# Performance work log

Measured on AMD Instinct MI355X. Metric: run time of the kernel, lower is better.

## Reference

```python
import jax, jax.numpy as jnp
import numpy as np

NB = 5  # frequency bands


def _ln(x, g, b, eps=1e-5):
    m = jnp.mean(x, axis=-1, keepdims=True)
    v = jnp.var(x, axis=-1, keepdims=True)
    return (x - m) / jnp.sqrt(v + eps) * g + b


def _graph_adj(x, adj_w, sw1, sb1, sw2, sb2, pos_factor, pos_enc):
    # x: [B, D, N] -> degree-normalized adjacency [B, N, N]
    d = x.shape[1]
    xt = jnp.swapaxes(x, 1, 2)  # [B, N, D]
    # concat-MLP first layer split: cat(xi, xj) @ W1 == xi @ W1[:d] + xj @ W1[d:]
    a = xt @ sw1[:d]
    bpart = xt @ sw1[d:]
    h = jax.nn.elu(a[:, :, None, :] + bpart[:, None, :, :] + sb1)  # [B, N, N, H]
    dyn = jax.nn.sigmoid(jnp.squeeze(h @ sw2, -1) + sb2)  # [B, N, N]
    static = jax.nn.softmax(adj_w, axis=-1)
    pos = jax.nn.softmax(pos_enc, axis=-1)
    comb = jax.nn.softmax(static + dyn + pos_factor * pos, axis=-1)
    deg = jnp.sum(comb, axis=-1)
    dis = (deg + 1e-8) ** -0.5
    return dis[:, :, None] * comb * dis[:, None, :]


def _gcn(x, adj, w, b):
    # x: [B, D, N], adj: [B, N, N] -> [B, D_out, N]
    xt = jnp.swapaxes(x, 1, 2)
    out = jnp.einsum('bij,bjd->bid', adj, xt) @ w + b
    return jnp.swapaxes(out, 1, 2)


def _mha(x, qkv_w, qkv_b, ow, ob, nh=4):
    B, S, D = x.shape
    dh = D // nh
    q, k, v = jnp.split(x @ qkv_w + qkv_b, 3, axis=-1)
    q = q.reshape(B, S, nh, dh)
    k = k.reshape(B, S, nh, dh)
    v = v.reshape(B, S, nh, dh)
    att = jax.nn.softmax(jnp.einsum('bihd,bjhd->bhij', q, k) / float(np.sqrt(dh)), axis=-1)
    o = jnp.einsum('bhij,bjhd->bihd', att, v).reshape(B, S, D)
    return o @ ow + ob


def setup_inputs():
    key = jax.random.key(0)
    B, D, N = 16, 256, 64
    ks = iter(jax.random.split(key, 40))

    def rn(shape, s=0.05):
        return jax.random.normal(next(ks), shape, dtype=jnp.float32) * s

    eyeN = jnp.eye(N, dtype=jnp.float32)
    return dict(
        feature=jax.random.normal(next(ks), (B, NB * D, 1, N), dtype=jnp.float32),
        l_adj_w=jnp.tile(eyeN[None], (NB, 1, 1)),
        l_sim_w1=rn((NB, 2 * D, D)), l_sim_b1=jnp.zeros((NB, D), jnp.float32),
        l_sim_w2=rn((NB, D, 1)), l_sim_b2=jnp.zeros((NB, 1), jnp.float32),
        l_pos_factor=jnp.full((NB,), 0.5, jnp.float32),
        l_pos_enc=jnp.tile(eyeN[None], (NB, 1, 1)),
        l_gcn_w=rn((NB, D, D)), l_gcn_b=jnp.zeros((NB, D), jnp.float32),
        g_adj_w=jnp.eye(NB, dtype=jnp.float32),
        g_sim_w1=rn((2 * D, D)), g_sim_b1=jnp.zeros((D,), jnp.float32),
        g_sim_w2=rn((D, 1)), g_sim_b2=jnp.zeros((1,), jnp.float32),
        g_pos_factor=jnp.float32(0.5),
        g_pos_enc=jnp.eye(NB, dtype=jnp.float32),
        g_gcn_w=rn((D, D)), g_gcn_b=jnp.zeros((D,), jnp.float32),
        qkv_w=rn((D, 3 * D)), qkv_b=jnp.zeros((3 * D,), jnp.float32),
        attn_ow=rn((D, D)), attn_ob=jnp.zeros((D,), jnp.float32),
        ln1_g=jnp.ones((D,), jnp.float32), ln1_b=jnp.zeros((D,), jnp.float32),
        ln2_g=jnp.ones((D,), jnp.float32), ln2_b=jnp.zeros((D,), jnp.float32),
        mlp_w1=rn((D, 4 * D)), mlp_b1=jnp.zeros((4 * D,), jnp.float32),
        mlp_w2=rn((4 * D, D)), mlp_b2=jnp.zeros((D,), jnp.float32),
        imp_w=rn((NB, N, 1)), imp_b=jnp.zeros((NB, 1), jnp.float32),
    )


def reference(feature, l_adj_w, l_sim_w1, l_sim_b1, l_sim_w2, l_sim_b2,
              l_pos_factor, l_pos_enc, l_gcn_w, l_gcn_b,
              g_adj_w, g_sim_w1, g_sim_b1, g_sim_w2, g_sim_b2,
              g_pos_factor, g_pos_enc, g_gcn_w, g_gcn_b,
              qkv_w, qkv_b, attn_ow, attn_ob,
              ln1_g, ln1_b, ln2_g, ln2_b,
              mlp_w1, mlp_b1, mlp_w2, mlp_b2,
              imp_w, imp_b):
    B = feature.shape[0]
    D = l_gcn_w.shape[-1]
    N = feature.shape[-1]
    # [B, 5*D, 1, N] -> [5, B, D, N] band-major
    x5 = jnp.moveaxis(feature.reshape(B, NB, D, N), 1, 0)
    # per-band local graphs + GCNs (vmapped over the 5 bands)
    local_adj = jax.vmap(_graph_adj)(x5, l_adj_w, l_sim_w1, l_sim_b1,
                                     l_sim_w2, l_sim_b2, l_pos_factor, l_pos_enc)
    local_out = jax.vmap(_gcn)(x5, local_adj, l_gcn_w, l_gcn_b)  # [5, B, D, N]
    scale_nodes = jnp.moveaxis(jnp.mean(local_out, axis=-1), 0, 1)  # [B, 5, D]
    # cross-band attention block (pre: MHA + residual + LN, then MLP + residual + LN)
    attn = _mha(scale_nodes, qkv_w, qkv_b, attn_ow, attn_ob)
    h1 = _ln(scale_nodes + attn, ln1_g, ln1_b)
    mlp = jax.nn.gelu(h1 @ mlp_w1 + mlp_b1, approximate=False) @ mlp_w2 + mlp_b2
    se = _ln(h1 + mlp, ln2_g, ln2_b)  # [B, 5, D]
    # global scale graph over the 5 band nodes
    xg = jnp.swapaxes(se, 1, 2)  # [B, D, 5]
    g_adj = _graph_adj(xg, g_adj_w, g_sim_w1, g_sim_b1, g_sim_w2, g_sim_b2,
                       g_pos_factor, g_pos_enc)
    g_out = jnp.swapaxes(_gcn(xg, g_adj, g_gcn_w, g_gcn_b), 1, 2)  # [B, 5, D]
    # modulate each local band feature by its global scale vector
    enh = local_out * jnp.moveaxis(g_out, 1, 0)[..., None]  # [5, B, D, N]
    # per-band importance projection over channels: [5, B, D, 1]
    out5 = jnp.einsum('kbdn,kno->kbdo', enh, imp_w) + imp_b[:, None, None, :]
    output = jnp.moveaxis(out5, 0, 1).reshape(B, NB * D, 1, 1)
    return output, g_adj, jnp.moveaxis(local_out, 0, 1)
```

## Files before the change

### kernel.cpp

```cpp
#include <hip/hip_runtime.h>
#include <hip/hip_bf16.h>

#define NBANDS 5
#define BATCH  16
#define DIM    256
#define NNODE  64
#define SEQ    5
#define NHEAD  4
#define DHEAD  64

typedef __hip_bfloat16 bf16;
typedef unsigned short ushort_t;
typedef __attribute__((ext_vector_type(8))) short short8;
typedef __attribute__((ext_vector_type(4))) float float4v;

__device__ __forceinline__ float bu2f(ushort_t u){
    bf16 h = *reinterpret_cast<bf16*>(&u);
    return __bfloat162float(h);
}
__device__ __forceinline__ ushort_t f2bu(float x){
    bf16 h = __float2bfloat16(x);
    return *reinterpret_cast<ushort_t*>(&h);
}

__global__ void __launch_bounds__(256) k_head(
    const float* __restrict__ l_adj_w, const float* __restrict__ l_pos_enc,
    const float* __restrict__ l_pf,
    const float* __restrict__ g_adj_w, const float* __restrict__ g_pos_enc,
    const float* __restrict__ g_pf,
    float* __restrict__ sbase, float* __restrict__ gbase,
    const float* __restrict__ w1, const float* __restrict__ gw,
    ushort_t* __restrict__ w1bt, ushort_t* __restrict__ gwbt,
    const float* __restrict__ feat,
    ushort_t* __restrict__ xtb, ushort_t* __restrict__ xtT)
{
    int blk = blockIdx.x;
    int tid = threadIdx.x;
    __shared__ ushort_t tile[64][65];

    if (blk < 80) {
        int r = blk*4 + (tid>>6);
        int k = r >> 6, i = r & 63;
        int t = tid & 63;
        float aw = l_adj_w[(k*NNODE + i)*NNODE + t];
        float pe = l_pos_enc[(k*NNODE + i)*NNODE + t];
        float m1 = aw, m2 = pe;
        for (int o=32;o>0;o>>=1){ m1 = fmaxf(m1, __shfl_xor(m1,o,64)); m2 = fmaxf(m2, __shfl_xor(m2,o,64)); }
        float e1 = __expf(aw-m1), e2 = __expf(pe-m2);
        float s1=e1, s2=e2;
        for (int o=32;o>0;o>>=1){ s1 += __shfl_xor(s1,o,64); s2 += __shfl_xor(s2,o,64); }
        float pf = l_pf[k];
        sbase[(k*NNODE+i)*NNODE + t] = e1/s1 + pf*(e2/s2);
    } else if (blk == 80) {
        if (tid < NBANDS) {
            int i = tid;
            float r1[NBANDS], r2[NBANDS];
            float m1=-1e30f, m2=-1e30f;
            for (int j=0;j<NBANDS;j++){
                r1[j]=g_adj_w[i*NBANDS+j]; r2[j]=g_pos_enc[i*NBANDS+j];
                m1=fmaxf(m1,r1[j]); m2=fmaxf(m2,r2[j]);
            }
            float s1=0.f,s2=0.f;
            for (int j=0;j<NBANDS;j++){ r1[j]=__expf(r1[j]-m1); r2[j]=__expf(r2[j]-m2); s1+=r1[j]; s2+=r2[j]; }
            float pf = g_pf[0];
            for (int j=0;j<NBANDS;j++) gbase[i*NBANDS+j] = r1[j]/s1 + pf*(r2[j]/s2);
        }
    } else if (blk < 321) {
        int idx = blk - 81;
        int inst = idx >> 4;
        int t = idx & 15;
        int r0 = (t>>2)*64, c0 = (t&3)*64;
        const float* src; ushort_t* dst;
        if (inst < 10){
            int k = inst>>1, half = inst&1;
            src = w1  + ((size_t)k*512 + half*256)*256;
            dst = w1bt+ ((size_t)k*512 + half*256)*256;
        } else {
            int k = inst-10;
            src = gw  + (size_t)k*65536;
            dst = gwbt+ (size_t)k*65536;
        }
        int jj = tid & 63, i4 = tid >> 6;
        for (int p=0;p<16;p++){
            int i = p*4 + i4;
            tile[i][jj] = f2bu(src[(size_t)(r0+i)*256 + c0 + jj]);
        }
        __syncthreads();
        for (int p=0;p<16;p++){
            int i = p*4 + i4;
            dst[(size_t)(c0+i)*256 + r0 + jj] = tile[jj][i];
        }
    } else {
        int idx = blk - 321;
        int k = idx >> 6;
        int b = (idx >> 2) & 15;
        int dt = idx & 3;
        const float* src = feat + ((size_t)b*NBANDS*DIM + (size_t)k*DIM)*NNODE;
        ushort_t* dst = xtb + (size_t)(k*BATCH+b)*NNODE*DIM;
        ushort_t* dstT = xtT + (size_t)(k*BATCH+b)*DIM*NNODE;
        for (int u=0; u<16; ++u){
            int i = dt*4096 + u*256 + tid;
            dstT[i] = f2bu(src[i]);
        }
        for (int r=0;r<16;r++){
            int dp = r*4 + (tid>>6);
            int n  = tid & 63;
            tile[dp][n] = f2bu(src[(size_t)(dt*64+dp)*NNODE + n]);
        }
        __syncthreads();
        for (int r=0;r<16;r++){
            int n  = r*4 + (tid>>6);
            int dp = tid & 63;
            dst[(size_t)n*DIM + dt*64 + dp] = tile[dp][n];
        }
    }
}

__global__ void __launch_bounds__(256) k_ab_mfma(const ushort_t* __restrict__ xtb,
                        const ushort_t* __restrict__ w1bt, const float* __restrict__ b1,
                        ushort_t* __restrict__ aab, ushort_t* __restrict__ bbb)
{
    int blk = blockIdx.x;
    int kband = blk / (BATCH*8);
    int b = (blk/8) % BATCH;
    int nblk = blk & 7;
    int tid = threadIdx.x;
    int wave = tid>>6, lane = tid&63;
    int c16 = lane & 15, quad = lane >> 4;
    int m0 = wave*16;
    size_t rowbase = (size_t)(kband*BATCH+b)*NNODE;
    const ushort_t* Aptr = xtb + (rowbase + m0 + c16)*DIM + quad*8;
    const ushort_t* Bbase = w1bt + (size_t)kband*512*DIM;
    int ncol0 = nblk*64;
    const ushort_t* Bptr0 = Bbase + (size_t)(ncol0 +  0 + c16)*DIM + quad*8;
    const ushort_t* Bptr1 = Bbase + (size_t)(ncol0 + 16 + c16)*DIM + quad*8;
    const ushort_t* Bptr2 = Bbase + (size_t)(ncol0 + 32 + c16)*DIM + quad*8;
    const ushort_t* Bptr3 = Bbase + (size_t)(ncol0 + 48 + c16)*DIM + quad*8;
    float4v acc0 = {0.f,0.f,0.f,0.f}, acc1 = acc0, acc2 = acc0, acc3 = acc0;
    #pragma unroll
    for (int ks=0; ks<8; ++ks){
        short8 a  = *reinterpret_cast<const short8*>(Aptr  + ks*32);
        short8 b0 = *reinterpret_cast<const short8*>(Bptr0 + ks*32);
        short8 b1v= *reinterpret_cast<const short8*>(Bptr1 + ks*32);
        short8 b2 = *reinterpret_cast<const short8*>(Bptr2 + ks*32);
        short8 b3 = *reinterpret_cast<const short8*>(Bptr3 + ks*32);
        acc0 = __builtin_amdgcn_mfma_f32_16x16x32_bf16(a, b0, acc0, 0,0,0);
        acc1 = __builtin_amdgcn_mfma_f32_16x16x32_bf16(a, b1v, acc1, 0,0,0);
        acc2 = __builtin_amdgcn_mfma_f32_16x16x32_bf16(a, b2, acc2, 0,0,0);
        acc3 = __builtin_amdgcn_mfma_f32_16x16x32_bf16(a, b3, acc3, 0,0,0);
    }
    int half = nblk >> 2;
    int cbase = (nblk & 3)*64;
    ushort_t* dst = half ? bbb : aab;
    float4v accs[4] = {acc0, acc1, acc2, acc3};
    #pragma unroll
    for (int nt=0; nt<4; ++nt){
        int cg = cbase + nt*16 + c16;
        float bias = half ? 0.f : b1[kband*DIM + cg];
        #pragma unroll
        for (int r=0;r<4;r++){
            int m = m0 + quad*4 + r;
            dst[(rowbase + m)*DIM + cg] = f2bu(accs[nt][r] + bias);
        }
    }
}

__global__ void __launch_bounds__(256) k_dyn_comb(const ushort_t* __restrict__ aab,
                           const ushort_t* __restrict__ bbb,
                           const float* __restrict__ w2, const float* __restrict__ b2arr,
                           const float* __restrict__ sbase,
                           ushort_t* __restrict__ combb)
{
    int blk = blockIdx.x;
    int k = blk / (BATCH*16);
    int b = (blk / 16) % BATCH;
    int i0 = (blk % 16) * 4;
    int kb = k*BATCH + b;
    __shared__ ushort_t bs[64][260];
    __shared__ float arows[4][DIM];
    __shared__ float w2s[DIM];
    int tid = threadIdx.x;
    int wave = tid >> 6, lane = tid & 63;
    const ushort_t* bsrc = bbb + (size_t)kb*NNODE*DIM;
    for (int u=0; u<16; ++u){
        int idx = u*1024 + tid*4;
        int row = idx >> 8, col = idx & 255;
        *reinterpret_cast<ushort4*>(&bs[row][col]) =
            *reinterpret_cast<const ushort4*>(&bsrc[(size_t)row*DIM + col]);
    }
    for (int r=0;r<4;r++) arows[r][tid] = bu2f(aab[((size_t)kb*NNODE + i0 + r)*DIM + tid]);
    w2s[tid] = w2[k*DIM + tid];
    __syncthreads();

    int i = i0 + wave;
    float acc = 0.f;
    #pragma unroll 4
    for (int dd=0; dd<64; ++dd){
        ushort4 bv = *reinterpret_cast<const ushort4*>(&bs[lane][dd*4]);
        float4 av = *reinterpret_cast<const float4*>(&arows[wave][dd*4]);
        float4 wv = *reinterpret_cast<const float4*>(&w2s[dd*4]);
        float v0 = av.x + bu2f(bv.x);
        float v1 = av.y + bu2f(bv.y);
        float v2 = av.z + bu2f(bv.z);
        float v3 = av.w + bu2f(bv.w);
        float e0 = (v0>0.f)? v0 : (__expf(v0)-1.f);
        float e1 = (v1>0.f)? v1 : (__expf(v1)-1.f);
        float e2 = (v2>0.f)? v2 : (__expf(v2)-1.f);
        float e3 = (v3>0.f)? v3 : (__expf(v3)-1.f);
        acc += e0*wv.x + e1*wv.y + e2*wv.z + e3*wv.w;
    }
    float sb2 = b2arr[k];
    float sg = 1.f/(1.f + __expf(-(acc + sb2)));
    float val = sbase[(k*NNODE + i)*NNODE + lane] + sg;
    float m = val;
    for (int o=32;o>0;o>>=1) m = fmaxf(m, __shfl_xor(m,o,64));
    float e = __expf(val - m);
    float s = e;
    for (int o=32;o>0;o>>=1) s += __shfl_xor(s,o,64);
    combb[((size_t)kb*NNODE + i)*NNODE + lane] = f2bu(e/s);
}

__global__ void __launch_bounds__(256) k_y_mfma(const ushort_t* __restrict__ combb,
                       const ushort_t* __restrict__ xtT,
                       ushort_t* __restrict__ yb)
{
    int blk = blockIdx.x;
    int kband = blk / (BATCH*4);
    int b = (blk/4) % BATCH;
    int nblk = blk & 3;
    int tid = threadIdx.x;
    int wave = tid>>6, lane = tid&63;
    int c16 = lane & 15, quad = lane >> 4;
    int m0 = wave*16;
    int kb = kband*BATCH + b;
    const ushort_t* Aptr = combb + ((size_t)kb*NNODE + m0 + c16)*NNODE + quad*8;
    const ushort_t* Bbase = xtT + (size_t)kb*DIM*NNODE;
    int ncol0 = nblk*64;
    const ushort_t* Bptr0 = Bbase + (size_t)(ncol0 +  0 + c16)*NNODE + quad*8;
    const ushort_t* Bptr1 = Bbase + (size_t)(ncol0 + 16 + c16)*NNODE + quad*8;
    const ushort_t* Bptr2 = Bbase + (size_t)(ncol0 + 32 + c16)*NNODE + quad*8;
    const ushort_t* Bptr3 = Bbase + (size_t)(ncol0 + 48 + c16)*NNODE + quad*8;
    float4v acc0 = {0.f,0.f,0.f,0.f}, acc1 = acc0, acc2 = acc0, acc3 = acc0;
    #pragma unroll
    for (int ks=0; ks<2; ++ks){
        short8 a  = *reinterpret_cast<const short8*>(Aptr  + ks*32);
        short8 b0 = *reinterpret_cast<const short8*>(Bptr0 + ks*32);
        short8 b1v= *reinterpret_cast<const short8*>(Bptr1 + ks*32);
        short8 b2 = *reinterpret_cast<const short8*>(Bptr2 + ks*32);
        short8 b3 = *reinterpret_cast<const short8*>(Bptr3 + ks*32);
        acc0 = __builtin_amdgcn_mfma_f32_16x16x32_bf16(a, b0, acc0, 0,0,0);
        acc1 = __builtin_amdgcn_mfma_f32_16x16x32_bf16(a, b1v, acc1, 0,0,0);
        acc2 = __builtin_amdgcn_mfma_f32_16x16x32_bf16(a, b2, acc2, 0,0,0);
        acc3 = __builtin_amdgcn_mfma_f32_16x16x32_bf16(a, b3, acc3, 0,0,0);
    }
    size_t rowbase = (size_t)kb*NNODE;
    float4v accs[4] = {acc0, acc1, acc2, acc3};
    #pragma unroll
    for (int nt=0; nt<4; ++nt){
        int cg = ncol0 + nt*16 + c16;
        #pragma unroll
        for (int r=0;r<4;r++){
            int m = m0 + quad*4 + r;
            yb[(rowbase + m)*DIM + cg] = f2bu(accs[nt][r]);
        }
    }
}

__global__ void __launch_bounds__(256) k_gcn_mfma(const ushort_t* __restrict__ yb,
                         const ushort_t* __restrict__ gwbt, const float* __restrict__ gb,
                         const float* __restrict__ imp_w,
                         float* __restrict__ out_local,
                         float* __restrict__ scalew, float* __restrict__ impw)
{
    int blk = blockIdx.x;
    int kband = blk / (BATCH*4);
    int b = (blk/4) % BATCH;
    int nblk = blk & 3;
    int tid = threadIdx.x;
    int wave = tid>>6, lane = tid&63;
    int c16 = lane & 15, quad = lane >> 4;
    int m0 = wave*16;
    int kb = kband*BATCH + b;
    __shared__ float iw_s[NNODE];
    __shared__ float sred[4][64];
    __shared__ float ired[4][64];
    if (tid < NNODE) iw_s[tid] = imp_w[kband*NNODE + tid];
    const ushort_t* Aptr = yb + ((size_t)kb*NNODE + m0 + c16)*DIM + quad*8;
    const ushort_t* Bbase = gwbt + (size_t)kband*DIM*DIM;
    int ncol0 = nblk*64;
    const ushort_t* Bptr0 = Bbase + (size_t)(ncol0 +  0 + c16)*DIM + quad*8;
    const ushort_t* Bptr1 = Bbase + (size_t)(ncol0 + 16 + c16)*DIM + quad*8;
    const ushort_t* Bptr2 = Bbase + (size_t)(ncol0 + 32 + c16)*DIM + quad*8;
    const ushort_t* Bptr3 = Bbase + (size_t)(ncol0 + 48 + c16)*DIM + quad*8;
    float4v acc0 = {0.f,0.f,0.f,0.f}, acc1 = acc0, acc2 = acc0, acc3 = acc0;
    #pragma unroll
    for (int ks=0; ks<8; ++ks){
        short8 a  = *reinterpret_cast<const short8*>(Aptr  + ks*32);
        short8 b0 = *reinterpret_cast<const short8*>(Bptr0 + ks*32);
        short8 b1v= *reinterpret_cast<const short8*>(Bptr1 + ks*32);
        short8 b2 = *reinterpret_cast<const short8*>(Bptr2 + ks*32);
        short8 b3 = *reinterpret_cast<const short8*>(Bptr3 + ks*32);
        acc0 = __builtin_amdgcn_mfma_f32_16x16x32_bf16(a, b0, acc0, 0,0,0);
        acc1 = __builtin_amdgcn_mfma_f32_16x16x32_bf16(a, b1v, acc1, 0,0,0);
        acc2 = __builtin_amdgcn_mfma_f32_16x16x32_bf16(a, b2, acc2, 0,0,0);
        acc3 = __builtin_amdgcn_mfma_f32_16x16x32_bf16(a, b3, acc3, 0,0,0);
    }
    __syncthreads();
    float4v accs[4] = {acc0, acc1, acc2, acc3};
    #pragma unroll
    for (int nt=0; nt<4; ++nt){
        int cg = ncol0 + nt*16 + c16;
        float bias = gb[kband*DIM + cg];
        float v0 = accs[nt][0]+bias, v1 = accs[nt][1]+bias, v2 = accs[nt][2]+bias, v3 = accs[nt][3]+bias;
        float4 v = make_float4(v0, v1, v2, v3);
        float* dst = out_local + ((size_t)(b*NBANDS + kband)*DIM + cg)*NNODE + m0 + quad*4;
        *reinterpret_cast<float4*>(dst) = v;
        int nb = m0 + quad*4;
        float s  = v0 + v1 + v2 + v3;
        float di = v0*iw_s[nb] + v1*iw_s[nb+1] + v2*iw_s[nb+2] + v3*iw_s[nb+3];
        s  += __shfl_xor(s, 16, 64);  s  += __shfl_xor(s, 32, 64);
        di += __shfl_xor(di, 16, 64); di += __shfl_xor(di, 32, 64);
        if (quad == 0){
            sred[wave][nt*16 + c16] = s;
            ired[wave][nt*16 + c16] = di;
        }
    }
    __syncthreads();
    if (tid < 64){
        float s  = sred[0][tid] + sred[1][tid] + sred[2][tid] + sred[3][tid];
        float di = ired[0][tid] + ired[1][tid] + ired[2][tid] + ired[3][tid];
        size_t o = ((size_t)b*SEQ + kband)*DIM + ncol0 + tid;
        scalew[o] = s * (1.f/64.f);
        impw[o]   = di;
    }
}

template<int COLS, int SLICES>
__global__ void __launch_bounds__(256) k_gemv(const float* __restrict__ x, const float* __restrict__ w,
                       const float* __restrict__ bias, float* __restrict__ out,
                       int K, int N, int act)
{
    int chunks = N / COLS;
    int row = blockIdx.x / chunks;
    int n0 = (blockIdx.x % chunks) * COLS;
    int c = threadIdx.x % COLS, s = threadIdx.x / COLS;
    __shared__ float xs[1024];
    __shared__ float part[SLICES][COLS];
    for (int i = threadIdx.x; i < K; i += 256) xs[i] = x[(size_t)row*K + i];
    __syncthreads();
    int klen = K / SLICES;
    const float* wp = w + (size_t)(s*klen)*N + n0 + c;
    const float* xp = xs + s*klen;
    float acc = 0.f;
    #pragma unroll 8
    for (int i = 0; i < klen; ++i) acc += xp[i] * wp[(size_t)i*N];
    part[s][c] = acc;
    __syncthreads();
    if (s == 0){
        float v = bias[n0+c];
        #pragma unroll
        for (int q=0;q<SLICES;q++) v += part[q][c];
        if (act) v = 0.5f*v*(1.f + erff(v*0.70710678118654752f));
        out[(size_t)row*N + n0 + c] = v;
    }
}

__global__ void __launch_bounds__(256) k_projattn(const float* __restrict__ qkvw,
                        const float* __restrict__ ow, const float* __restrict__ ob,
                        float* __restrict__ projw)
{
    int row = blockIdx.x / 4;
    int n0 = (blockIdx.x % 4) * 64;
    int b = row / SEQ, i = row % SEQ;
    int tid = threadIdx.x;
    int h = tid >> 6, l = tid & 63;
    __shared__ float xs[DIM];
    __shared__ float part[4][64];
    const float* base = qkvw + (size_t)b*SEQ*3*DIM;
    float qv = base[(size_t)i*3*DIM + h*DHEAD + l];
    float pj[SEQ];
    #pragma unroll
    for (int j=0;j<SEQ;j++){
        float p = qv * base[(size_t)j*3*DIM + DIM + h*DHEAD + l];
        for (int o=32;o>0;o>>=1) p += __shfl_xor(p,o,64);
        pj[j] = p * 0.125f;
    }
    float m = pj[0];
    #pragma unroll
    for (int j=1;j<SEQ;j++) m = fmaxf(m, pj[j]);
    float ssum = 0.f;
    #pragma unroll
    for (int j=0;j<SEQ;j++){ pj[j] = __expf(pj[j]-m); ssum += pj[j]; }
    float inv = 1.f/ssum;
    float o = 0.f;
    #pragma unroll
    for (int j=0;j<SEQ;j++) o += pj[j]*inv * base[(size_t)j*3*DIM + 2*DIM + h*DHEAD + l];
    xs[tid] = o;
    __syncthreads();
    int c = tid & 63, s = tid >> 6;
    const float* wp = ow + (size_t)(s*64)*DIM + n0 + c;
    const float* xp = xs + s*64;
    float acc = 0.f;
    #pragma unroll 8
    for (int k=0;k<64;++k) acc += xp[k] * wp[(size_t)k*DIM];
    part[s][c] = acc;
    __syncthreads();
    if (s == 0){
        projw[(size_t)row*DIM + n0 + c] = ob[n0+c] + part[0][c]+part[1][c]+part[2][c]+part[3][c];
    }
}

__device__ __forceinline__ float block_ln(float v, int tid, float* red, float g, float bln)
{
    float s = v;
    for (int o=32;o>0;o>>=1) s += __shfl_xor(s,o,64);
    int wave = tid>>6, lane = tid&63;
    if (lane==0) red[wave] = s;
    __syncthreads();
    float mean = (red[0]+red[1]+red[2]+red[3]) * (1.f/DIM);
    float c = v - mean;
    float q = c*c;
    for (int o=32;o>0;o>>=1) q += __shfl_xor(q,o,64);
    __syncthreads();
    if (lane==0) red[wave] = q;
    __syncthreads();
    float var = (red[0]+red[1]+red[2]+red[3]) * (1.f/DIM);
    return c * rsqrtf(var + 1e-5f) * g + bln;
}

__global__ void __launch_bounds__(256) k_mlp1_ln(const float* __restrict__ projw,
                         const float* __restrict__ scalew,
                         const float* __restrict__ ln1_g, const float* __restrict__ ln1_b,
                         const float* __restrict__ w1, const float* __restrict__ b1,
                         float* __restrict__ h1w, float* __restrict__ mhw)
{
    int row = blockIdx.x / 16;
    int n0 = (blockIdx.x % 16) * 64;
    int tid = threadIdx.x;
    __shared__ float xs[DIM];
    __shared__ float red[4];
    __shared__ float part[4][64];
    float v = projw[(size_t)row*DIM + tid] + scalew[(size_t)row*DIM + tid];
    float h = block_ln(v, tid, red, ln1_g[tid], ln1_b[tid]);
    xs[tid] = h;
    if ((blockIdx.x % 16) == 0) h1w[(size_t)row*DIM + tid] = h;
    __syncthreads();
    int c = tid & 63, s = tid >> 6;
    const float* wp = w1 + (size_t)(s*64)*1024 + n0 + c;
    const float* xp = xs + s*64;
    float acc = 0.f;
    #pragma unroll 8
    for (int i=0;i<64;++i) acc += xp[i] * wp[(size_t)i*1024];
    part[s][c] = acc;
    __syncthreads();
    if (s == 0){
        float o = b1[n0+c] + part[0][c] + part[1][c] + part[2][c] + part[3][c];
        o = 0.5f*o*(1.f + erff(o*0.70710678118654752f));
        mhw[(size_t)row*1024 + n0 + c] = o;
    }
}

__global__ void __launch_bounds__(256) k_gab_ln(const float* __restrict__ m2w,
                        const float* __restrict__ h1w,
                        const float* __restrict__ ln2_g, const float* __restrict__ ln2_b,
                        const float* __restrict__ gw1, const float* __restrict__ gb1,
                        float* __restrict__ sew, float* __restrict__ gaw, float* __restrict__ gbw)
{
    int row = blockIdx.x / 4;
    int n0 = (blockIdx.x % 4) * 64;
    int tid = threadIdx.x;
    __shared__ float xs[DIM];
    __shared__ float red[4];
    __shared__ float partA[4][64];
    __shared__ float partB[4][64];
    float v = m2w[(size_t)row*DIM + tid] + h1w[(size_t)row*DIM + tid];
    float h = block_ln(v, tid, red, ln2_g[tid], ln2_b[tid]);
    xs[tid] = h;
    if ((blockIdx.x % 4) == 0) sew[(size_t)row*DIM + tid] = h;
    __syncthreads();
    int c = tid & 63, s = tid >> 6;
    const float* wpA = gw1 + (size_t)(s*64)*DIM + n0 + c;
    const float* wpB = wpA + (size_t)DIM*DIM;
    const float* xp = xs + s*64;
    float aA = 0.f, aB = 0.f;
    #pragma unroll 8
    for (int i=0;i<64;++i){
        float xv = xp[i];
        aA += xv * wpA[(size_t)i*DIM];
        aB += xv * wpB[(size_t)i*DIM];
    }
    partA[s][c] = aA;
    partB[s][c] = aB;
    __syncthreads();
    if (s == 0){
        gaw[(size_t)row*DIM + n0 + c] = gb1[n0+c] + partA[0][c]+partA[1][c]+partA[2][c]+partA[3][c];
        gbw[(size_t)row*DIM + n0 + c] = partB[0][c]+partB[1][c]+partB[2][c]+partB[3][c];
    }
}

__global__ void __launch_bounds__(256) k_goutfin(const float* __restrict__ gaw,
                        const float* __restrict__ gbw,
                        const float* __restrict__ gw2, const float* __restrict__ gb2,
                        const float* __restrict__ gbase,
                        const float* __restrict__ sew,
                        const float* __restrict__ ggw, const float* __restrict__ ggb,
                        const float* __restrict__ impw, const float* __restrict__ imp_b,
                        float* __restrict__ out0, float* __restrict__ out_gadj)
{
    int row = blockIdx.x / 4;
    int n0 = (blockIdx.x % 4) * 64;
    int b = row / SEQ, i = row % SEQ;
    int tid = threadIdx.x;
    int wave = tid >> 6, lane = tid & 63;
    __shared__ float dyn_s[SEQ];
    __shared__ float xs[DIM];
    __shared__ float part[4][64];
    for (int j = wave; j < SEQ; j += 4){
        const float* gar = gaw + (size_t)row*DIM;
        const float* gbr = gbw + ((size_t)b*SEQ + j)*DIM;
        float acc = 0.f;
        #pragma unroll
        for (int m=0;m<4;m++){
            int dd = lane + m*64;
            float v = gar[dd] + gbr[dd];
            float e = (v>0.f) ? v : (__expf(v)-1.f);
            acc += e * gw2[dd];
        }
        for (int o=32;o>0;o>>=1) acc += __shfl_xor(acc,o,64);
        if (lane==0) dyn_s[j] = acc;
    }
    __syncthreads();
    float gc[SEQ];
    {
        float sb2 = gb2[0];
        float m = -1e30f;
        #pragma unroll
        for (int j=0;j<SEQ;j++){
            float sg = 1.f/(1.f+__expf(-(dyn_s[j]+sb2)));
            gc[j] = gbase[i*SEQ+j] + sg;
            m = fmaxf(m, gc[j]);
        }
        float ssum=0.f;
        #pragma unroll
        for (int j=0;j<SEQ;j++){ gc[j]=__expf(gc[j]-m); ssum+=gc[j]; }
        float inv = 1.f/ssum;
        #pragma unroll
        for (int j=0;j<SEQ;j++) gc[j] *= inv;
    }
    if (n0 == 0 && tid < SEQ) out_gadj[((size_t)b*SEQ+i)*SEQ + tid] = gc[tid];
    float t = 0.f;
    #pragma unroll
    for (int j=0;j<SEQ;j++) t += gc[j]*sew[((size_t)b*SEQ + j)*DIM + tid];
    xs[tid] = t;
    __syncthreads();
    int c = tid & 63, s = tid >> 6;
    const float* wp = ggw + (size_t)(s*64)*DIM + n0 + c;
    const float* xp = xs + s*64;
    float acc = 0.f;
    #pragma unroll 8
    for (int k=0;k<64;++k) acc += xp[k] * wp[(size_t)k*DIM];
    part[s][c] = acc;
    __syncthreads();
    if (s == 0){
        float g = ggb[n0+c] + part[0][c]+part[1][c]+part[2][c]+part[3][c];
        size_t o = (size_t)row*DIM + n0 + c;
        out0[o] = g * impw[o] + imp_b[i];
    }
}

extern "C" void kernel_launch(void* const* d_in, const int* in_sizes, int n_in,
                              void* d_out, int out_size, void* d_ws, size_t ws_size,
                              hipStream_t stream)
{
    const float* feature      = (const float*)d_in[0];
    const float* l_adj_w      = (const float*)d_in[1];
    const float* l_sim_w1     = (const float*)d_in[2];
    const float* l_sim_b1     = (const float*)d_in[3];
    const float* l_sim_w2     = (const float*)d_in[4];
    const float* l_sim_b2     = (const float*)d_in[5];
    const float* l_pos_factor = (const float*)d_in[6];
    const float* l_pos_enc    = (const float*)d_in[7];
    const float* l_gcn_w      = (const float*)d_in[8];
    const float* l_gcn_b      = (const float*)d_in[9];
    const float* g_adj_w      = (const float*)d_in[10];
    const float* g_sim_w1     = (const float*)d_in[11];
    const float* g_sim_b1     = (const float*)d_in[12];
    const float* g_sim_w2     = (const float*)d_in[13];
    const float* g_sim_b2     = (const float*)d_in[14];
    const float* g_pos_factor = (const float*)d_in[15];
    const float* g_pos_enc    = (const float*)d_in[16];
    const float* g_gcn_w      = (const float*)d_in[17];
    const float* g_gcn_b      = (const float*)d_in[18];
    const float* qkv_w        = (const float*)d_in[19];
    const float* qkv_b        = (const float*)d_in[20];
    const float* attn_ow      = (const float*)d_in[21];
    const float* attn_ob      = (const float*)d_in[22];
    const float* ln1_g        = (const float*)d_in[23];
    const float* ln1_b        = (const float*)d_in[24];
    const float* ln2_g        = (const float*)d_in[25];
    const float* ln2_b        = (const float*)d_in[26];
    const float* mlp_w1       = (const float*)d_in[27];
    const float* mlp_b1       = (const float*)d_in[28];
    const float* mlp_w2       = (const float*)d_in[29];
    const float* mlp_b2       = (const float*)d_in[30];
    const float* imp_w        = (const float*)d_in[31];
    const float* imp_b        = (const float*)d_in[32];

    float* out0      = (float*)d_out;
    float* out_gadj  = out0 + (size_t)BATCH*NBANDS*DIM;
    float* out_local = out_gadj + (size_t)BATCH*NBANDS*NBANDS;

    const size_t BIG = (size_t)NBANDS*BATCH*NNODE*DIM;
    ushort_t* xtb   = (ushort_t*)d_ws;
    ushort_t* aab   = xtb + BIG;
    ushort_t* bbb   = aab + BIG;
    ushort_t* xtT   = bbb + BIG;
    ushort_t* yb    = aab;
    ushort_t* w1bt  = xtT + BIG;
    ushort_t* gwbt  = w1bt + (size_t)NBANDS*512*DIM;
    ushort_t* combb = gwbt + (size_t)NBANDS*DIM*DIM;
    float* fp = (float*)(combb + (size_t)NBANDS*BATCH*NNODE*NNODE);
    float* sbase  = fp; fp += NBANDS*NNODE*NNODE;
    float* gbase  = fp; fp += 32;
    float* scalew = fp; fp += BATCH*SEQ*DIM;
    float* impw   = fp; fp += BATCH*SEQ*DIM;
    float* qkvw   = fp; fp += BATCH*SEQ*3*DIM;
    float* projw  = fp; fp += BATCH*SEQ*DIM;
    float* h1w    = fp; fp += BATCH*SEQ*DIM;
    float* mhw    = fp; fp += BATCH*SEQ*4*DIM;
    float* m2w    = fp; fp += BATCH*SEQ*DIM;
    float* sew    = fp; fp += BATCH*SEQ*DIM;
    float* gaw    = fp; fp += BATCH*SEQ*DIM;
    float* gbw    = fp; fp += BATCH*SEQ*DIM;

    const int ROWS = BATCH*SEQ;

    k_head<<<641, 256, 0, stream>>>(l_adj_w, l_pos_enc, l_pos_factor,
                                    g_adj_w, g_pos_enc, g_pos_factor,
                                    sbase, gbase,
                                    l_sim_w1, l_gcn_w, w1bt, gwbt,
                                    feature, xtb, xtT);
    k_ab_mfma<<<NBANDS*BATCH*8, 256, 0, stream>>>(xtb, w1bt, l_sim_b1, aab, bbb);
    k_dyn_comb<<<NBANDS*BATCH*16, 256, 0, stream>>>(aab, bbb, l_sim_w2, l_sim_b2, sbase, combb);
    k_y_mfma<<<NBANDS*BATCH*4, 256, 0, stream>>>(combb, xtT, yb);
    k_gcn_mfma<<<NBANDS*BATCH*4, 256, 0, stream>>>(yb, gwbt, l_gcn_b, imp_w,
                                                   out_local, scalew, impw);
    k_gemv<64,4><<<ROWS*12, 256, 0, stream>>>(scalew, qkv_w, qkv_b, qkvw, 256, 768, 0);
    k_projattn<<<ROWS*4, 256, 0, stream>>>(qkvw, attn_ow, attn_ob, projw);
    k_mlp1_ln<<<ROWS*16, 256, 0, stream>>>(projw, scalew, ln1_g, ln1_b, mlp_w1, mlp_b1, h1w, mhw);
    k_gemv<32,8><<<ROWS*8, 256, 0, stream>>>(mhw, mlp_w2, mlp_b2, m2w, 1024, 256, 0);
    k_gab_ln<<<ROWS*4, 256, 0, stream>>>(m2w, h1w, ln2_g, ln2_b, g_sim_w1, g_sim_b1, sew, gaw, gbw);
    k_goutfin<<<ROWS*4, 256, 0, stream>>>(gaw, gbw, g_sim_w2, g_sim_b2, gbase,
                                          sew, g_gcn_w, g_gcn_b, impw, imp_b,
                                          out0, out_gadj);
}
```

Before: 218.3 us.

## Fuse all stages into one cooperative persistent kernel with grid syncs

Replaces the chain of eleven separate kernel launches with a single cooperative kernel of 256 blocks. Each stage's work units are looped over by the persistent blocks, with grid-wide synchronization between stages. Shared memory is carved from a common buffer, and a fallback path launches per-stage wrapper kernels if the cooperative launch fails. This aims to remove per-launch overhead and inter-kernel idle gaps, at the cost of grid-barrier latency and a fixed block count that may underfill large stages.

Result: slower. 592.1 us (+171.2%).

```diff
diff --git a/kernel.cpp b/kernel.cpp
--- a/kernel.cpp
+++ b/kernel.cpp
@@ -1,5 +1,6 @@
 #include <hip/hip_runtime.h>
 #include <hip/hip_bf16.h>
+#include <hip/hip_cooperative_groups.h>
 
 #define NBANDS 5
 #define BATCH  16
@@ -9,6 +10,8 @@
 #define NHEAD  4
 #define DHEAD  64
 
+namespace cg = cooperative_groups;
+
 typedef __hip_bfloat16 bf16;
 typedef unsigned short ushort_t;
 typedef __attribute__((ext_vector_type(8))) short short8;
@@ -23,47 +26,67 @@
     return *reinterpret_cast<ushort_t*>(&h);
 }
 
-__global__ void __launch_bounds__(256) k_head(
-    const float* __restrict__ l_adj_w, const float* __restrict__ l_pos_enc,
-    const float* __restrict__ l_pf,
-    const float* __restrict__ g_adj_w, const float* __restrict__ g_pos_enc,
-    const float* __restrict__ g_pf,
-    float* __restrict__ sbase, float* __restrict__ gbase,
-    const float* __restrict__ w1, const float* __restrict__ gw,
-    ushort_t* __restrict__ w1bt, ushort_t* __restrict__ gwbt,
-    const float* __restrict__ feat,
-    ushort_t* __restrict__ xtb, ushort_t* __restrict__ xtT)
-{
-    int blk = blockIdx.x;
-    int tid = threadIdx.x;
-    __shared__ ushort_t tile[64][65];
-
+struct P {
+    const float *l_adj_w, *l_pos_enc, *l_pf, *g_adj_w, *g_pos_enc, *g_pf;
+    const float *w1, *gw, *feat, *b1, *w2, *b2arr, *gb;
+    const float *imp_w, *imp_b;
+    const float *qkv_w, *qkv_b, *attn_ow, *attn_ob;
+    const float *ln1_g, *ln1_b, *mlp_w1, *mlp_b1, *mlp_w2, *mlp_b2, *ln2_g, *ln2_b;
+    const float *g_sim_w1, *g_sim_b1, *g_sim_w2, *g_sim_b2, *g_gcn_w, *g_gcn_b;
+    float *sbase, *gbase;
+    ushort_t *w1bt, *gwbt, *xtb, *xtT, *aab, *bbb, *yb, *combb;
+    float *scalew, *impw, *qkvw, *projw, *h1w, *mhw, *m2w, *sew, *gaw, *gbw;
+    float *out0, *out_gadj, *out_local;
+};
+
+__device__ __forceinline__ float block_ln(float v, int tid, float* red, float g, float bln)
+{
+    float s = v;
+    for (int o=32;o>0;o>>=1) s += __shfl_xor(s,o,64);
+    int wave = tid>>6, lane = tid&63;
+    if (lane==0) red[wave] = s;
+    __syncthreads();
+    float mean = (red[0]+red[1]+red[2]+red[3]) * (1.f/DIM);
+    float c = v - mean;
+    float q = c*c;
+    for (int o=32;o>0;o>>=1) q += __shfl_xor(q,o,64);
+    __syncthreads();
+    if (lane==0) red[wave] = q;
+    __syncthreads();
+    float var = (red[0]+red[1]+red[2]+red[3]) * (1.f/DIM);
+    return c * rsqrtf(var + 1e-5f) * g + bln;
+}
+
+
+__device__ __forceinline__ void st_head_unit(const P& p, int blk, int tid, char* smem)
+{
+    ushort_t (*tile)[65] = (ushort_t(*)[65])smem;
     if (blk < 80) {
         int r = blk*4 + (tid>>6);
         int k = r >> 6, i = r & 63;
         int t = tid & 63;
-        float aw = l_adj_w[(k*NNODE + i)*NNODE + t];
-        float pe = l_pos_enc[(k*NNODE + i)*NNODE + t];
+        float aw = p.l_adj_w[(k*NNODE + i)*NNODE + t];
+        float pe = p.l_pos_enc[(k*NNODE + i)*NNODE + t];
         float m1 = aw, m2 = pe;
         for (int o=32;o>0;o>>=1){ m1 = fmaxf(m1, __shfl_xor(m1,o,64)); m2 = fmaxf(m2, __shfl_xor(m2,o,64)); }
         float e1 = __expf(aw-m1), e2 = __expf(pe-m2);
         float s1=e1, s2=e2;
         for (int o=32;o>0;o>>=1){ s1 += __shfl_xor(s1,o,64); s2 += __shfl_xor(s2,o,64); }
-        float pf = l_pf[k];
-        sbase[(k*NNODE+i)*NNODE + t] = e1/s1 + pf*(e2/s2);
+        float pf = p.l_pf[k];
+        p.sbase[(k*NNODE+i)*NNODE + t] = e1/s1 + pf*(e2/s2);
     } else if (blk == 80) {
         if (tid < NBANDS) {
             int i = tid;
             float r1[NBANDS], r2[NBANDS];
             float m1=-1e30f, m2=-1e30f;
             for (int j=0;j<NBANDS;j++){
-                r1[j]=g_adj_w[i*NBANDS+j]; r2[j]=g_pos_enc[i*NBANDS+j];
+                r1[j]=p.g_adj_w[i*NBANDS+j]; r2[j]=p.g_pos_enc[i*NBANDS+j];
                 m1=fmaxf(m1,r1[j]); m2=fmaxf(m2,r2[j]);
             }
             float s1=0.f,s2=0.f;
             for (int j=0;j<NBANDS;j++){ r1[j]=__expf(r1[j]-m1); r2[j]=__expf(r2[j]-m2); s1+=r1[j]; s2+=r2[j]; }
-            float pf = g_pf[0];
-            for (int j=0;j<NBANDS;j++) gbase[i*NBANDS+j] = r1[j]/s1 + pf*(r2[j]/s2);
+            float pf = p.g_pf[0];
+            for (int j=0;j<NBANDS;j++) p.gbase[i*NBANDS+j] = r1[j]/s1 + pf*(r2[j]/s2);
         }
     } else if (blk < 321) {
         int idx = blk - 81;
@@ -73,21 +96,21 @@
         const float* src; ushort_t* dst;
         if (inst < 10){
             int k = inst>>1, half = inst&1;
-            src = w1  + ((size_t)k*512 + half*256)*256;
-            dst = w1bt+ ((size_t)k*512 + half*256)*256;
+            src = p.w1  + ((size_t)k*512 + half*256)*256;
+            dst = p.w1bt+ ((size_t)k*512 + half*256)*256;
         } else {
             int k = inst-10;
-            src = gw  + (size_t)k*65536;
-            dst = gwbt+ (size_t)k*65536;
+            src = p.gw  + (size_t)k*65536;
+            dst = p.gwbt+ (size_t)k*65536;
         }
         int jj = tid & 63, i4 = tid >> 6;
-        for (int p=0;p<16;p++){
-            int i = p*4 + i4;
+        for (int q=0;q<16;q++){
+            int i = q*4 + i4;
             tile[i][jj] = f2bu(src[(size_t)(r0+i)*256 + c0 + jj]);
         }
         __syncthreads();
-        for (int p=0;p<16;p++){
-            int i = p*4 + i4;
+        for (int q=0;q<16;q++){
+            int i = q*4 + i4;
             dst[(size_t)(c0+i)*256 + r0 + jj] = tile[jj][i];
         }
     } else {
@@ -95,9 +118,9 @@
         int k = idx >> 6;
         int b = (idx >> 2) & 15;
         int dt = idx & 3;
-        const float* src = feat + ((size_t)b*NBANDS*DIM + (size_t)k*DIM)*NNODE;
-        ushort_t* dst = xtb + (size_t)(k*BATCH+b)*NNODE*DIM;
-        ushort_t* dstT = xtT + (size_t)(k*BATCH+b)*DIM*NNODE;
+        const float* src = p.feat + ((size_t)b*NBANDS*DIM + (size_t)k*DIM)*NNODE;
+        ushort_t* dst = p.xtb + (size_t)(k*BATCH+b)*NNODE*DIM;
+        ushort_t* dstT = p.xtT + (size_t)(k*BATCH+b)*DIM*NNODE;
         for (int u=0; u<16; ++u){
             int i = dt*4096 + u*256 + tid;
             dstT[i] = f2bu(src[i]);
@@ -116,21 +139,17 @@
     }
 }
 
-__global__ void __launch_bounds__(256) k_ab_mfma(const ushort_t* __restrict__ xtb,
-                        const ushort_t* __restrict__ w1bt, const float* __restrict__ b1,
-                        ushort_t* __restrict__ aab, ushort_t* __restrict__ bbb)
-{
-    int blk = blockIdx.x;
+__device__ __forceinline__ void st_ab_unit(const P& p, int blk, int tid)
+{
+    int wave = tid>>6, lane = tid&63;
+    int c16 = lane & 15, quad = lane >> 4;
+    int m0 = wave*16;
     int kband = blk / (BATCH*8);
     int b = (blk/8) % BATCH;
     int nblk = blk & 7;
-    int tid = threadIdx.x;
-    int wave = tid>>6, lane = tid&63;
-    int c16 = lane & 15, quad = lane >> 4;
-    int m0 = wave*16;
     size_t rowbase = (size_t)(kband*BATCH+b)*NNODE;
-    const ushort_t* Aptr = xtb + (rowbase + m0 + c16)*DIM + quad*8;
-    const ushort_t* Bbase = w1bt + (size_t)kband*512*DIM;
+    const ushort_t* Aptr = p.xtb + (rowbase + m0 + c16)*DIM + quad*8;
+    const ushort_t* Bbase = p.w1bt + (size_t)kband*512*DIM;
     int ncol0 = nblk*64;
     const ushort_t* Bptr0 = Bbase + (size_t)(ncol0 +  0 + c16)*DIM + quad*8;
     const ushort_t* Bptr1 = Bbase + (size_t)(ncol0 + 16 + c16)*DIM + quad*8;
@@ -151,45 +170,39 @@
     }
     int half = nblk >> 2;
     int cbase = (nblk & 3)*64;
-    ushort_t* dst = half ? bbb : aab;
+    ushort_t* dst = half ? p.bbb : p.aab;
     float4v accs[4] = {acc0, acc1, acc2, acc3};
     #pragma unroll
     for (int nt=0; nt<4; ++nt){
-        int cg = cbase + nt*16 + c16;
-        float bias = half ? 0.f : b1[kband*DIM + cg];
+        int cg2 = cbase + nt*16 + c16;
+        float bias = half ? 0.f : p.b1[kband*DIM + cg2];
         #pragma unroll
         for (int r=0;r<4;r++){
             int m = m0 + quad*4 + r;
-            dst[(rowbase + m)*DIM + cg] = f2bu(accs[nt][r] + bias);
-        }
-    }
-}
-
-__global__ void __launch_bounds__(256) k_dyn_comb(const ushort_t* __restrict__ aab,
-                           const ushort_t* __restrict__ bbb,
-                           const float* __restrict__ w2, const float* __restrict__ b2arr,
-                           const float* __restrict__ sbase,
-                           ushort_t* __restrict__ combb)
-{
-    int blk = blockIdx.x;
+            dst[(rowbase + m)*DIM + cg2] = f2bu(accs[nt][r] + bias);
+        }
+    }
+}
+
+__device__ __forceinline__ void st_dyn_unit(const P& p, int blk, int tid, char* smem)
+{
+    ushort_t (*bs)[260] = (ushort_t(*)[260])smem;
+    float (*arows)[DIM] = (float(*)[DIM])(smem + 33280);
+    float* w2s = (float*)(smem + 33280 + 4096);
+    int wave = tid >> 6, lane = tid & 63;
     int k = blk / (BATCH*16);
     int b = (blk / 16) % BATCH;
     int i0 = (blk % 16) * 4;
     int kb = k*BATCH + b;
-    __shared__ ushort_t bs[64][260];
-    __shared__ float arows[4][DIM];
-    __shared__ float w2s[DIM];
-    int tid = threadIdx.x;
-    int wave = tid >> 6, lane = tid & 63;
-    const ushort_t* bsrc = bbb + (size_t)kb*NNODE*DIM;
+    const ushort_t* bsrc = p.bbb + (size_t)kb*NNODE*DIM;
     for (int u=0; u<16; ++u){
         int idx = u*1024 + tid*4;
         int row = idx >> 8, col = idx & 255;
         *reinterpret_cast<ushort4*>(&bs[row][col]) =
             *reinterpret_cast<const ushort4*>(&bsrc[(size_t)row*DIM + col]);
     }
-    for (int r=0;r<4;r++) arows[r][tid] = bu2f(aab[((size_t)kb*NNODE + i0 + r)*DIM + tid]);
-    w2s[tid] = w2[k*DIM + tid];
+    for (int r=0;r<4;r++) arows[r][tid] = bu2f(p.aab[((size_t)kb*NNODE + i0 + r)*DIM + tid]);
+    w2s[tid] = p.w2[k*DIM + tid];
     __syncthreads();
 
     int i = i0 + wave;
@@ -209,32 +222,28 @@
         float e3 = (v3>0.f)? v3 : (__expf(v3)-1.f);
         acc += e0*wv.x + e1*wv.y + e2*wv.z + e3*wv.w;
     }
-    float sb2 = b2arr[k];
+    float sb2 = p.b2arr[k];
     float sg = 1.f/(1.f + __expf(-(acc + sb2)));
-    float val = sbase[(k*NNODE + i)*NNODE + lane] + sg;
+    float val = p.sbase[(k*NNODE + i)*NNODE + lane] + sg;
     float m = val;
     for (int o=32;o>0;o>>=1) m = fmaxf(m, __shfl_xor(m,o,64));
     float e = __expf(val - m);
     float s = e;
     for (int o=32;o>0;o>>=1) s += __shfl_xor(s,o,64);
-    combb[((size_t)kb*NNODE + i)*NNODE + lane] = f2bu(e/s);
-}
-
-__global__ void __launch_bounds__(256) k_y_mfma(const ushort_t* __restrict__ combb,
-                       const ushort_t* __restrict__ xtT,
-                       ushort_t* __restrict__ yb)
-{
-    int blk = blockIdx.x;
+    p.combb[((size_t)kb*NNODE + i)*NNODE + lane] = f2bu(e/s);
+}
+
+__device__ __forceinline__ void st_y_unit(const P& p, int blk, int tid)
+{
+    int wave = tid>>6, lane = tid&63;
+    int c16 = lane & 15, quad = lane >> 4;
+    int m0 = wave*16;
     int kband = blk / (BATCH*4);
     int b = (blk/4) % BATCH;
     int nblk = blk & 3;
-    int tid = threadIdx.x;
-    int wave = tid>>6, lane = tid&63;
-    int c16 = lane & 15, quad = lane >> 4;
-    int m0 = wave*16;
     int kb = kband*BATCH + b;
-    const ushort_t* Aptr = combb + ((size_t)kb*NNODE + m0 + c16)*NNODE + quad*8;
-    const ushort_t* Bbase = xtT + (size_t)kb*DIM*NNODE;
+    const ushort_t* Aptr = p.combb + ((size_t)kb*NNODE + m0 + c16)*NNODE + quad*8;
+    const ushort_t* Bbase = p.xtT + (size_t)kb*DIM*NNODE;
     int ncol0 = nblk*64;
     const ushort_t* Bptr0 = Bbase + (size_t)(ncol0 +  0 + c16)*NNODE + quad*8;
     const ushort_t* Bptr1 = Bbase + (size_t)(ncol0 + 16 + c16)*NNODE + quad*8;
@@ -257,36 +266,30 @@
     float4v accs[4] = {acc0, acc1, acc2, acc3};
     #pragma unroll
     for (int nt=0; nt<4; ++nt){
-        int cg = ncol0 + nt*16 + c16;
+        int cg2 = ncol0 + nt*16 + c16;
         #pragma unroll
         for (int r=0;r<4;r++){
             int m = m0 + quad*4 + r;
-            yb[(rowbase + m)*DIM + cg] = f2bu(accs[nt][r]);
-        }
-    }
-}
-
-__global__ void __launch_bounds__(256) k_gcn_mfma(const ushort_t* __restrict__ yb,
-                         const ushort_t* __restrict__ gwbt, const float* __restrict__ gb,
-                         const float* __restrict__ imp_w,
-                         float* __restrict__ out_local,
-                         float* __restrict__ scalew, float* __restrict__ impw)
-{
-    int blk = blockIdx.x;
+            p.yb[(rowbase + m)*DIM + cg2] = f2bu(accs[nt][r]);
+        }
+    }
+}
+
+__device__ __forceinline__ void st_gcn_unit(const P& p, int blk, int tid, char* smem)
+{
+    float* iw_s = (float*)smem;
+    float (*sred)[64] = (float(*)[64])(smem + 256);
+    float (*ired)[64] = (float(*)[64])(smem + 256 + 1024);
+    int wave = tid>>6, lane = tid&63;
+    int c16 = lane & 15, quad = lane >> 4;
+    int m0 = wave*16;
     int kband = blk / (BATCH*4);
     int b = (blk/4) % BATCH;
     int nblk = blk & 3;
-    int tid = threadIdx.x;
-    int wave = tid>>6, lane = tid&63;
-    int c16 = lane & 15, quad = lane >> 4;
-    int m0 = wave*16;
     int kb = kband*BATCH + b;
-    __shared__ float iw_s[NNODE];
-    __shared__ float sred[4][64];
-    __shared__ float ired[4][64];
-    if (tid < NNODE) iw_s[tid] = imp_w[kband*NNODE + tid];
-    const ushort_t* Aptr = yb + ((size_t)kb*NNODE + m0 + c16)*DIM + quad*8;
-    const ushort_t* Bbase = gwbt + (size_t)kband*DIM*DIM;
+    if (tid < NNODE) iw_s[tid] = p.imp_w[kband*NNODE + tid];
+    const ushort_t* Aptr = p.yb + ((size_t)kb*NNODE + m0 + c16)*DIM + quad*8;
+    const ushort_t* Bbase = p.gwbt + (size_t)kband*DIM*DIM;
     int ncol0 = nblk*64;
     const ushort_t* Bptr0 = Bbase + (size_t)(ncol0 +  0 + c16)*DIM + quad*8;
     const ushort_t* Bptr1 = Bbase + (size_t)(ncol0 + 16 + c16)*DIM + quad*8;
@@ -309,11 +312,11 @@
     float4v accs[4] = {acc0, acc1, acc2, acc3};
     #pragma unroll
     for (int nt=0; nt<4; ++nt){
-        int cg = ncol0 + nt*16 + c16;
-        float bias = gb[kband*DIM + cg];
+        int cg2 = ncol0 + nt*16 + c16;
+        float bias = p.gb[kband*DIM + cg2];
         float v0 = accs[nt][0]+bias, v1 = accs[nt][1]+bias, v2 = accs[nt][2]+bias, v3 = accs[nt][3]+bias;
         float4 v = make_float4(v0, v1, v2, v3);
-        float* dst = out_local + ((size_t)(b*NBANDS + kband)*DIM + cg)*NNODE + m0 + quad*4;
+        float* dst = p.out_local + ((size_t)(b*NBANDS + kband)*DIM + cg2)*NNODE + m0 + quad*4;
         *reinterpret_cast<float4*>(dst) = v;
         int nb = m0 + quad*4;
         float s  = v0 + v1 + v2 + v3;
@@ -330,60 +333,49 @@
         float s  = sred[0][tid] + sred[1][tid] + sred[2][tid] + sred[3][tid];
         float di = ired[0][tid] + ired[1][tid] + ired[2][tid] + ired[3][tid];
         size_t o = ((size_t)b*SEQ + kband)*DIM + ncol0 + tid;
-        scalew[o] = s * (1.f/64.f);
-        impw[o]   = di;
-    }
-}
-
-template<int COLS, int SLICES>
-__global__ void __launch_bounds__(256) k_gemv(const float* __restrict__ x, const float* __restrict__ w,
-                       const float* __restrict__ bias, float* __restrict__ out,
-                       int K, int N, int act)
-{
-    int chunks = N / COLS;
-    int row = blockIdx.x / chunks;
-    int n0 = (blockIdx.x % chunks) * COLS;
-    int c = threadIdx.x % COLS, s = threadIdx.x / COLS;
-    __shared__ float xs[1024];
-    __shared__ float part[SLICES][COLS];
-    for (int i = threadIdx.x; i < K; i += 256) xs[i] = x[(size_t)row*K + i];
-    __syncthreads();
-    int klen = K / SLICES;
-    const float* wp = w + (size_t)(s*klen)*N + n0 + c;
-    const float* xp = xs + s*klen;
+        p.scalew[o] = s * (1.f/64.f);
+        p.impw[o]   = di;
+    }
+}
+
+__device__ __forceinline__ void st_qkv_unit(const P& p, int u, int tid, char* smem)
+{
+    float* xs = (float*)smem;
+    float (*part)[64] = (float(*)[64])(smem + 4096);
+    int c = tid & 63, s = tid >> 6;
+    int row = u / 12;
+    int n0 = (u % 12) * 64;
+    xs[tid] = p.scalew[(size_t)row*DIM + tid];
+    __syncthreads();
+    const float* wp = p.qkv_w + (size_t)(s*64)*768 + n0 + c;
+    const float* xp = xs + s*64;
     float acc = 0.f;
     #pragma unroll 8
-    for (int i = 0; i < klen; ++i) acc += xp[i] * wp[(size_t)i*N];
+    for (int i = 0; i < 64; ++i) acc += xp[i] * wp[(size_t)i*768];
     part[s][c] = acc;
     __syncthreads();
     if (s == 0){
-        float v = bias[n0+c];
-        #pragma unroll
-        for (int q=0;q<SLICES;q++) v += part[q][c];
-        if (act) v = 0.5f*v*(1.f + erff(v*0.70710678118654752f));
-        out[(size_t)row*N + n0 + c] = v;
-    }
-}
-
-__global__ void __launch_bounds__(256) k_projattn(const float* __restrict__ qkvw,
-                        const float* __restrict__ ow, const float* __restrict__ ob,
-                        float* __restrict__ projw)
-{
-    int row = blockIdx.x / 4;
-    int n0 = (blockIdx.x % 4) * 64;
+        p.qkvw[(size_t)row*768 + n0 + c] = p.qkv_b[n0+c] + part[0][c]+part[1][c]+part[2][c]+part[3][c];
+    }
+}
+
+__device__ __forceinline__ void st_projattn_unit(const P& p, int u, int tid, char* smem)
+{
+    float* xs = (float*)smem;
+    float (*part)[64] = (float(*)[64])(smem + 1024);
+    int h = tid >> 6, l = tid & 63;
+    int c = tid & 63, s = tid >> 6;
+    int row = u / 4;
+    int n0 = (u % 4) * 64;
     int b = row / SEQ, i = row % SEQ;
-    int tid = threadIdx.x;
-    int h = tid >> 6, l = tid & 63;
-    __shared__ float xs[DIM];
-    __shared__ float part[4][64];
-    const float* base = qkvw + (size_t)b*SEQ*3*DIM;
+    const float* base = p.qkvw + (size_t)b*SEQ*3*DIM;
     float qv = base[(size_t)i*3*DIM + h*DHEAD + l];
     float pj[SEQ];
     #pragma unroll
     for (int j=0;j<SEQ;j++){
-        float p = qv * base[(size_t)j*3*DIM + DIM + h*DHEAD + l];
-        for (int o=32;o>0;o>>=1) p += __shfl_xor(p,o,64);
-        pj[j] = p * 0.125f;
+        float pr = qv * base[(size_t)j*3*DIM + DIM + h*DHEAD + l];
+        for (int o=32;o>0;o>>=1) pr += __shfl_xor(pr,o,64);
+        pj[j] = pr * 0.125f;
     }
     float m = pj[0];
     #pragma unroll
@@ -397,8 +389,7 @@
     for (int j=0;j<SEQ;j++) o += pj[j]*inv * base[(size_t)j*3*DIM + 2*DIM + h*DHEAD + l];
     xs[tid] = o;
     __syncthreads();
-    int c = tid & 63, s = tid >> 6;
-    const float* wp = ow + (size_t)(s*64)*DIM + n0 + c;
+    const float* wp = p.attn_ow + (size_t)(s*64)*DIM + n0 + c;
     const float* xp = xs + s*64;
     float acc = 0.f;
     #pragma unroll 8
@@ -406,47 +397,24 @@
     part[s][c] = acc;
     __syncthreads();
     if (s == 0){
-        projw[(size_t)row*DIM + n0 + c] = ob[n0+c] + part[0][c]+part[1][c]+part[2][c]+part[3][c];
-    }
-}
-
-__device__ __forceinline__ float block_ln(float v, int tid, float* red, float g, float bln)
-{
-    float s = v;
-    for (int o=32;o>0;o>>=1) s += __shfl_xor(s,o,64);
-    int wave = tid>>6, lane = tid&63;
-    if (lane==0) red[wave] = s;
-    __syncthreads();
-    float mean = (red[0]+red[1]+red[2]+red[3]) * (1.f/DIM);
-    float c = v - mean;
-    float q = c*c;
-    for (int o=32;o>0;o>>=1) q += __shfl_xor(q,o,64);
-    __syncthreads();
-    if (lane==0) red[wave] = q;
-    __syncthreads();
-    float var = (red[0]+red[1]+red[2]+red[3]) * (1.f/DIM);
-    return c * rsqrtf(var + 1e-5f) * g + bln;
-}
-
-__global__ void __launch_bounds__(256) k_mlp1_ln(const float* __restrict__ projw,
-                         const float* __restrict__ scalew,
-                         const float* __restrict__ ln1_g, const float* __restrict__ ln1_b,
-                         const float* __restrict__ w1, const float* __restrict__ b1,
-                         float* __restrict__ h1w, float* __restrict__ mhw)
-{
-    int row = blockIdx.x / 16;
-    int n0 = (blockIdx.x % 16) * 64;
-    int tid = threadIdx.x;
-    __shared__ float xs[DIM];
-    __shared__ float red[4];
-    __shared__ float part[4][64];
-    float v = projw[(size_t)row*DIM + tid] + scalew[(size_t)row*DIM + tid];
-    float h = block_ln(v, tid, red, ln1_g[tid], ln1_b[tid]);
+        p.projw[(size_t)row*DIM + n0 + c] = p.attn_ob[n0+c] + part[0][c]+part[1][c]+part[2][c]+part[3][c];
+    }
+}
+
+__device__ __forceinline__ void st_mlp1_unit(const P& p, int u, int tid, char* smem)
+{
+    float* xs = (float*)smem;
+    float* red = (float*)(smem + 1024);
+    float (*part)[64] = (float(*)[64])(smem + 1024 + 16);
+    int c = tid & 63, s = tid >> 6;
+    int row = u / 16;
+    int n0 = (u % 16) * 64;
+    float v = p.projw[(size_t)row*DIM + tid] + p.scalew[(size_t)row*DIM + tid];
+    float h = block_ln(v, tid, red, p.ln1_g[tid], p.ln1_b[tid]);
     xs[tid] = h;
-    if ((blockIdx.x % 16) == 0) h1w[(size_t)row*DIM + tid] = h;
-    __syncthreads();
-    int c = tid & 63, s = tid >> 6;
-    const float* wp = w1 + (size_t)(s*64)*1024 + n0 + c;
+    if ((u % 16) == 0) p.h1w[(size_t)row*DIM + tid] = h;
+    __syncthreads();
+    const float* wp = p.mlp_w1 + (size_t)(s*64)*1024 + n0 + c;
     const float* xp = xs + s*64;
     float acc = 0.f;
     #pragma unroll 8
@@ -454,32 +422,51 @@
     part[s][c] = acc;
     __syncthreads();
     if (s == 0){
-        float o = b1[n0+c] + part[0][c] + part[1][c] + part[2][c] + part[3][c];
+        float o = p.mlp_b1[n0+c] + part[0][c] + part[1][c] + part[2][c] + part[3][c];
         o = 0.5f*o*(1.f + erff(o*0.70710678118654752f));
-        mhw[(size_t)row*1024 + n0 + c] = o;
-    }
-}
-
-__global__ void __launch_bounds__(256) k_gab_ln(const float* __restrict__ m2w,
-                        const float* __restrict__ h1w,
-                        const float* __restrict__ ln2_g, const float* __restrict__ ln2_b,
-                        const float* __restrict__ gw1, const float* __restrict__ gb1,
-                        float* __restrict__ sew, float* __restrict__ gaw, float* __restrict__ gbw)
-{
-    int row = blockIdx.x / 4;
-    int n0 = (blockIdx.x % 4) * 64;
-    int tid = threadIdx.x;
-    __shared__ float xs[DIM];
-    __shared__ float red[4];
-    __shared__ float partA[4][64];
-    __shared__ float partB[4][64];
-    float v = m2w[(size_t)row*DIM + tid] + h1w[(size_t)row*DIM + tid];
-    float h = block_ln(v, tid, red, ln2_g[tid], ln2_b[tid]);
+        p.mhw[(size_t)row*1024 + n0 + c] = o;
+    }
+}
+
+__device__ __forceinline__ void st_mlp2_unit(const P& p, int u, int tid, char* smem)
+{
+    float* xs = (float*)smem;
+    float (*part)[32] = (float(*)[32])(smem + 4096);
+    int c = tid & 31, s = tid >> 5;
+    int row = u / 8;
+    int n0 = (u % 8) * 32;
+    for (int i = tid; i < 1024; i += 256) xs[i] = p.mhw[(size_t)row*1024 + i];
+    __syncthreads();
+    const float* wp = p.mlp_w2 + (size_t)(s*128)*DIM + n0 + c;
+    const float* xp = xs + s*128;
+    float acc = 0.f;
+    #pragma unroll 8
+    for (int i=0;i<128;++i) acc += xp[i] * wp[(size_t)i*DIM];
+    part[s][c] = acc;
+    __syncthreads();
+    if (s == 0){
+        float v = p.mlp_b2[n0+c];
+        #pragma unroll
+        for (int q=0;q<8;q++) v += part[q][c];
+        p.m2w[(size_t)row*DIM + n0 + c] = v;
+    }
+}
+
+__device__ __forceinline__ void st_gab_unit(const P& p, int u, int tid, char* smem)
+{
+    float* xs = (float*)smem;
+    float* red = (float*)(smem + 1024);
+    float (*partA)[64] = (float(*)[64])(smem + 1024 + 16);
+    float (*partB)[64] = (float(*)[64])(smem + 1024 + 16 + 1024);
+    int c = tid & 63, s = tid >> 6;
+    int row = u / 4;
+    int n0 = (u % 4) * 64;
+    float v = p.m2w[(size_t)row*DIM + tid] + p.h1w[(size_t)row*DIM + tid];
+    float h = block_ln(v, tid, red, p.ln2_g[tid], p.ln2_b[tid]);
     xs[tid] = h;
-    if ((blockIdx.x % 4) == 0) sew[(size_t)row*DIM + tid] = h;
-    __syncthreads();
-    int c = tid & 63, s = tid >> 6;
-    const float* wpA = gw1 + (size_t)(s*64)*DIM + n0 + c;
+    if ((u % 4) == 0) p.sew[(size_t)row*DIM + tid] = h;
+    __syncthreads();
+    const float* wpA = p.g_sim_w1 + (size_t)(s*64)*DIM + n0 + c;
     const float* wpB = wpA + (size_t)DIM*DIM;
     const float* xp = xs + s*64;
     float aA = 0.f, aB = 0.f;
@@ -493,38 +480,31 @@
     partB[s][c] = aB;
     __syncthreads();
     if (s == 0){
-        gaw[(size_t)row*DIM + n0 + c] = gb1[n0+c] + partA[0][c]+partA[1][c]+partA[2][c]+partA[3][c];
-        gbw[(size_t)row*DIM + n0 + c] = partB[0][c]+partB[1][c]+partB[2][c]+partB[3][c];
-    }
-}
-
-__global__ void __launch_bounds__(256) k_goutfin(const float* __restrict__ gaw,
-                        const float* __restrict__ gbw,
-                        const float* __restrict__ gw2, const float* __restrict__ gb2,
-                        const float* __restrict__ gbase,
-                        const float* __restrict__ sew,
-                        const float* __restrict__ ggw, const float* __restrict__ ggb,
-                        const float* __restrict__ impw, const float* __restrict__ imp_b,
-                        float* __restrict__ out0, float* __restrict__ out_gadj)
-{
-    int row = blockIdx.x / 4;
-    int n0 = (blockIdx.x % 4) * 64;
+        p.gaw[(size_t)row*DIM + n0 + c] = p.g_sim_b1[n0+c] + partA[0][c]+partA[1][c]+partA[2][c]+partA[3][c];
+        p.gbw[(size_t)row*DIM + n0 + c] = partB[0][c]+partB[1][c]+partB[2][c]+partB[3][c];
+    }
+}
+
+__device__ __forceinline__ void st_goutfin_unit(const P& p, int u, int tid, char* smem)
+{
+    float* dyn_s = (float*)smem;
+    float* xs = (float*)(smem + 64);
+    float (*part)[64] = (float(*)[64])(smem + 64 + 1024);
+    int wave = tid >> 6, lane = tid & 63;
+    int c = tid & 63, s = tid >> 6;
+    int row = u / 4;
+    int n0 = (u % 4) * 64;
     int b = row / SEQ, i = row % SEQ;
-    int tid = threadIdx.x;
-    int wave = tid >> 6, lane = tid & 63;
-    __shared__ float dyn_s[SEQ];
-    __shared__ float xs[DIM];
-    __shared__ float part[4][64];
     for (int j = wave; j < SEQ; j += 4){
-        const float* gar = gaw + (size_t)row*DIM;
-        const float* gbr = gbw + ((size_t)b*SEQ + j)*DIM;
+        const float* gar = p.gaw + (size_t)row*DIM;
+        const float* gbr = p.gbw + ((size_t)b*SEQ + j)*DIM;
         float acc = 0.f;
         #pragma unroll
         for (int m=0;m<4;m++){
             int dd = lane + m*64;
             float v = gar[dd] + gbr[dd];
             float e = (v>0.f) ? v : (__expf(v)-1.f);
-            acc += e * gw2[dd];
+            acc += e * p.g_sim_w2[dd];
         }
         for (int o=32;o>0;o>>=1) acc += __shfl_xor(acc,o,64);
         if (lane==0) dyn_s[j] = acc;
@@ -532,12 +512,12 @@
     __syncthreads();
     float gc[SEQ];
     {
-        float sb2 = gb2[0];
+        float sb2 = p.g_sim_b2[0];
         float m = -1e30f;
         #pragma unroll
         for (int j=0;j<SEQ;j++){
             float sg = 1.f/(1.f+__expf(-(dyn_s[j]+sb2)));
-            gc[j] = gbase[i*SEQ+j] + sg;
+            gc[j] = p.gbase[i*SEQ+j] + sg;
             m = fmaxf(m, gc[j]);
         }
         float ssum=0.f;
@@ -547,14 +527,13 @@
         #pragma unroll
         for (int j=0;j<SEQ;j++) gc[j] *= inv;
     }
-    if (n0 == 0 && tid < SEQ) out_gadj[((size_t)b*SEQ+i)*SEQ + tid] = gc[tid];
+    if (n0 == 0 && tid < SEQ) p.out_gadj[((size_t)b*SEQ+i)*SEQ + tid] = gc[tid];
     float t = 0.f;
     #pragma unroll
-    for (int j=0;j<SEQ;j++) t += gc[j]*sew[((size_t)b*SEQ + j)*DIM + tid];
+    for (int j=0;j<SEQ;j++) t += gc[j]*p.sew[((size_t)b*SEQ + j)*DIM + tid];
     xs[tid] = t;
     __syncthreads();
-    int c = tid & 63, s = tid >> 6;
-    const float* wp = ggw + (size_t)(s*64)*DIM + n0 + c;
+    const float* wp = p.g_gcn_w + (size_t)(s*64)*DIM + n0 + c;
     const float* xp = xs + s*64;
     float acc = 0.f;
     #pragma unroll 8
@@ -562,95 +541,135 @@
     part[s][c] = acc;
     __syncthreads();
     if (s == 0){
-        float g = ggb[n0+c] + part[0][c]+part[1][c]+part[2][c]+part[3][c];
+        float g = p.g_gcn_b[n0+c] + part[0][c]+part[1][c]+part[2][c]+part[3][c];
         size_t o = (size_t)row*DIM + n0 + c;
-        out0[o] = g * impw[o] + imp_b[i];
-    }
-}
+        p.out0[o] = g * p.impw[o] + p.imp_b[i];
+    }
+}
+
+__global__ void __launch_bounds__(256) k_mega(P p)
+{
+    cg::grid_group grid = cg::this_grid();
+    __shared__ __align__(16) char smem[38400];
+    int tid = threadIdx.x;
+    const int G = gridDim.x;
+
+    for (int blk = blockIdx.x; blk < 641; blk += G){ st_head_unit(p, blk, tid, smem); __syncthreads(); }
+    grid.sync();
+    for (int blk = blockIdx.x; blk < 640; blk += G){ st_ab_unit(p, blk, tid); }
+    grid.sync();
+    for (int blk = blockIdx.x; blk < 1280; blk += G){ st_dyn_unit(p, blk, tid, smem); __syncthreads(); }
+    grid.sync();
+    for (int blk = blockIdx.x; blk < 320; blk += G){ st_y_unit(p, blk, tid); }
+    grid.sync();
+    for (int blk = blockIdx.x; blk < 320; blk += G){ st_gcn_unit(p, blk, tid, smem); __syncthreads(); }
+    grid.sync();
+    for (int u = blockIdx.x; u < 960; u += G){ st_qkv_unit(p, u, tid, smem); __syncthreads(); }
+    grid.sync();
+    for (int u = blockIdx.x; u < 320; u += G){ st_projattn_unit(p, u, tid, smem); __syncthreads(); }
+    grid.sync();
+    for (int u = blockIdx.x; u < 1280; u += G){ st_mlp1_unit(p, u, tid, smem); __syncthreads(); }
+    grid.sync();
+    for (int u = blockIdx.x; u < 640; u += G){ st_mlp2_unit(p, u, tid, smem); __syncthreads(); }
+    grid.sync();
+    for (int u = blockIdx.x; u < 320; u += G){ st_gab_unit(p, u, tid, smem); __syncthreads(); }
+    grid.sync();
+    for (int u = blockIdx.x; u < 320; u += G){ st_goutfin_unit(p, u, tid, smem); __syncthreads(); }
+}
+
+__global__ void __launch_bounds__(256) k_f_head(P p){ __shared__ __align__(16) char smem[38400]; st_head_unit(p, blockIdx.x, threadIdx.x, smem); }
+__global__ void __launch_bounds__(256) k_f_ab(P p){ st_ab_unit(p, blockIdx.x, threadIdx.x); }
+__global__ void __launch_bounds__(256) k_f_dyn(P p){ __shared__ __align__(16) char smem[38400]; st_dyn_unit(p, blockIdx.x, threadIdx.x, smem); }
+__global__ void __launch_bounds__(256) k_f_y(P p){ st_y_unit(p, blockIdx.x, threadIdx.x); }
+__global__ void __launch_bounds__(256) k_f_gcn(P p){ __shared__ __align__(16) char smem[38400]; st_gcn_unit(p, blockIdx.x, threadIdx.x, smem); }
+__global__ void __launch_bounds__(256) k_f_qkv(P p){ __shared__ __align__(16) char smem[38400]; st_qkv_unit(p, blockIdx.x, threadIdx.x, smem); }
+__global__ void __launch_bounds__(256) k_f_projattn(P p){ __shared__ __align__(16) char smem[38400]; st_projattn_unit(p, blockIdx.x, threadIdx.x, smem); }
+__global__ void __launch_bounds__(256) k_f_mlp1(P p){ __shared__ __align__(16) char smem[38400]; st_mlp1_unit(p, blockIdx.x, threadIdx.x, smem); }
+__global__ void __launch_bounds__(256) k_f_mlp2(P p){ __shared__ __align__(16) char smem[38400]; st_mlp2_unit(p, blockIdx.x, threadIdx.x, smem); }
+__global__ void __launch_bounds__(256) k_f_gab(P p){ __shared__ __align__(16) char smem[38400]; st_gab_unit(p, blockIdx.x, threadIdx.x, smem); }
+__global__ void __launch_bounds__(256) k_f_goutfin(P p){ __shared__ __align__(16) char smem[38400]; st_goutfin_unit(p, blockIdx.x, threadIdx.x, smem); }
 
 extern "C" void kernel_launch(void* const* d_in, const int* in_sizes, int n_in,
                               void* d_out, int out_size, void* d_ws, size_t ws_size,
                               hipStream_t stream)
 {
-    const float* feature      = (const float*)d_in[0];
-    const float* l_adj_w      = (const float*)d_in[1];
-    const float* l_sim_w1     = (const float*)d_in[2];
-    const float* l_sim_b1     = (const float*)d_in[3];
-    const float* l_sim_w2     = (const float*)d_in[4];
-    const float* l_sim_b2     = (const float*)d_in[5];
-    const float* l_pos_factor = (const float*)d_in[6];
-    const float* l_pos_enc    = (const float*)d_in[7];
-    const float* l_gcn_w      = (const float*)d_in[8];
-    const float* l_gcn_b      = (const float*)d_in[9];
-    const float* g_adj_w      = (const float*)d_in[10];
-    const float* g_sim_w1     = (const float*)d_in[11];
-    const float* g_sim_b1     = (const float*)d_in[12];
-    const float* g_sim_w2     = (const float*)d_in[13];
-    const float* g_sim_b2     = (const float*)d_in[14];
-    const float* g_pos_factor = (const float*)d_in[15];
-    const float* g_pos_enc    = (const float*)d_in[16];
-    const float* g_gcn_w      = (const float*)d_in[17];
-    const float* g_gcn_b      = (const float*)d_in[18];
-    const float* qkv_w        = (const float*)d_in[19];
-    const float* qkv_b        = (const float*)d_in[20];
-    const float* attn_ow      = (const float*)d_in[21];
-    const float* attn_ob      = (const float*)d_in[22];
-    const float* ln1_g        = (const float*)d_in[23];
-    const float* ln1_b        = (const float*)d_in[24];
-    const float* ln2_g        = (const float*)d_in[25];
-    const float* ln2_b        = (const float*)d_in[26];
-    const float* mlp_w1       = (const float*)d_in[27];
-    const float* mlp_b1       = (const float*)d_in[28];
-    const float* mlp_w2       = (const float*)d_in[29];
-    const float* mlp_b2       = (const float*)d_in[30];
-    const float* imp_w        = (const float*)d_in[31];
-    const float* imp_b        = (const float*)d_in[32];
-
-    float* out0      = (float*)d_out;
-    float* out_gadj  = out0 + (size_t)BATCH*NBANDS*DIM;
-    float* out_local = out_gadj + (size_t)BATCH*NBANDS*NBANDS;
+    P prm;
+    prm.l_adj_w   = (const float*)d_in[1];
+    prm.w1        = (const float*)d_in[2];
+    prm.b1        = (const float*)d_in[3];
+    prm.w2        = (const float*)d_in[4];
+    prm.b2arr     = (const float*)d_in[5];
+    prm.l_pf      = (const float*)d_in[6];
+    prm.l_pos_enc = (const float*)d_in[7];
+    prm.gw        = (const float*)d_in[8];
+    prm.gb        = (const float*)d_in[9];
+    prm.g_adj_w   = (const float*)d_in[10];
+    prm.g_sim_w1  = (const float*)d_in[11];
+    prm.g_sim_b1  = (const float*)d_in[12];
+    prm.g_sim_w2  = (const float*)d_in[13];
+    prm.g_sim_b2  = (const float*)d_in[14];
+    prm.g_pf      = (const float*)d_in[15];
+    prm.g_pos_enc = (const float*)d_in[16];
+    prm.g_gcn_w   = (const float*)d_in[17];
+    prm.g_gcn_b   = (const float*)d_in[18];
+    prm.qkv_w     = (const float*)d_in[19];
+    prm.qkv_b     = (const float*)d_in[20];
+    prm.attn_ow   = (const float*)d_in[21];
+    prm.attn_ob   = (const float*)d_in[22];
+    prm.ln1_g     = (const float*)d_in[23];
+    prm.ln1_b     = (const float*)d_in[24];
+    prm.ln2_g     = (const float*)d_in[25];
+    prm.ln2_b     = (const float*)d_in[26];
+    prm.mlp_w1    = (const float*)d_in[27];
+    prm.mlp_b1    = (const float*)d_in[28];
+    prm.mlp_w2    = (const float*)d_in[29];
+    prm.mlp_b2    = (const float*)d_in[30];
+    prm.imp_w     = (const float*)d_in[31];
+    prm.imp_b     = (const float*)d_in[32];
+    prm.feat      = (const float*)d_in[0];
+
+    prm.out0      = (float*)d_out;
+    prm.out_gadj  = prm.out0 + (size_t)BATCH*NBANDS*DIM;
+    prm.out_local = prm.out_gadj + (size_t)BATCH*NBANDS*NBANDS;
 
     const size_t BIG = (size_t)NBANDS*BATCH*NNODE*DIM;
-    ushort_t* xtb   = (ushort_t*)d_ws;
-    ushort_t* aab   = xtb + BIG;
-    ushort_t* bbb   = aab + BIG;
-    ushort_t* xtT   = bbb + BIG;
-    ushort_t* yb    = aab;
-    ushort_t* w1bt  = xtT + BIG;
-    ushort_t* gwbt  = w1bt + (size_t)NBANDS*512*DIM;
-    ushort_t* combb = gwbt + (size_t)NBANDS*DIM*DIM;
-    float* fp = (float*)(combb + (size_t)NBANDS*BATCH*NNODE*NNODE);
-    float* sbase  = fp; fp += NBANDS*NNODE*NNODE;
-    float* gbase  = fp; fp += 32;
-    float* scalew = fp; fp += BATCH*SEQ*DIM;
-    float* impw   = fp; fp += BATCH*SEQ*DIM;
-    float* qkvw   = fp; fp += BATCH*SEQ*3*DIM;
-    float* projw  = fp; fp += BATCH*SEQ*DIM;
-    float* h1w    = fp; fp += BATCH*SEQ*DIM;
-    float* mhw    = fp; fp += BATCH*SEQ*4*DIM;
-    float* m2w    = fp; fp += BATCH*SEQ*DIM;
-    float* sew    = fp; fp += BATCH*SEQ*DIM;
-    float* gaw    = fp; fp += BATCH*SEQ*DIM;
-    float* gbw    = fp; fp += BATCH*SEQ*DIM;
-
-    const int ROWS = BATCH*SEQ;
-
-    k_head<<<641, 256, 0, stream>>>(l_adj_w, l_pos_enc, l_pos_factor,
-                                    g_adj_w, g_pos_enc, g_pos_factor,
-                                    sbase, gbase,
-                                    l_sim_w1, l_gcn_w, w1bt, gwbt,
-                                    feature, xtb, xtT);
-    k_ab_mfma<<<NBANDS*BATCH*8, 256, 0, stream>>>(xtb, w1bt, l_sim_b1, aab, bbb);
-    k_dyn_comb<<<NBANDS*BATCH*16, 256, 0, stream>>>(aab, bbb, l_sim_w2, l_sim_b2, sbase, combb);
-    k_y_mfma<<<NBANDS*BATCH*4, 256, 0, stream>>>(combb, xtT, yb);
-    k_gcn_mfma<<<NBANDS*BATCH*4, 256, 0, stream>>>(yb, gwbt, l_gcn_b, imp_w,
-                                                   out_local, scalew, impw);
-    k_gemv<64,4><<<ROWS*12, 256, 0, stream>>>(scalew, qkv_w, qkv_b, qkvw, 256, 768, 0);
-    k_projattn<<<ROWS*4, 256, 0, stream>>>(qkvw, attn_ow, attn_ob, projw);
-    k_mlp1_ln<<<ROWS*16, 256, 0, stream>>>(projw, scalew, ln1_g, ln1_b, mlp_w1, mlp_b1, h1w, mhw);
-    k_gemv<32,8><<<ROWS*8, 256, 0, stream>>>(mhw, mlp_w2, mlp_b2, m2w, 1024, 256, 0);
-    k_gab_ln<<<ROWS*4, 256, 0, stream>>>(m2w, h1w, ln2_g, ln2_b, g_sim_w1, g_sim_b1, sew, gaw, gbw);
-    k_goutfin<<<ROWS*4, 256, 0, stream>>>(gaw, gbw, g_sim_w2, g_sim_b2, gbase,
-                                          sew, g_gcn_w, g_gcn_b, impw, imp_b,
-                                          out0, out_gadj);
-}
+    prm.xtb   = (ushort_t*)d_ws;
+    prm.aab   = prm.xtb + BIG;
+    prm.bbb   = prm.aab + BIG;
+    prm.xtT   = prm.bbb + BIG;
+    prm.yb    = prm.aab;
+    prm.w1bt  = prm.xtT + BIG;
+    prm.gwbt  = prm.w1bt + (size_t)NBANDS*512*DIM;
+    prm.combb = prm.gwbt + (size_t)NBANDS*DIM*DIM;
+    float* fp = (float*)(prm.combb + (size_t)NBANDS*BATCH*NNODE*NNODE);
+    prm.sbase  = fp; fp += NBANDS*NNODE*NNODE;
+    prm.gbase  = fp; fp += 32;
+    prm.scalew = fp; fp += BATCH*SEQ*DIM;
+    prm.impw   = fp; fp += BATCH*SEQ*DIM;
+    prm.qkvw   = fp; fp += BATCH*SEQ*3*DIM;
+    prm.projw  = fp; fp += BATCH*SEQ*DIM;
+    prm.h1w    = fp; fp += BATCH*SEQ*DIM;
+    prm.mhw    = fp; fp += BATCH*SEQ*4*DIM;
+    prm.m2w    = fp; fp += BATCH*SEQ*DIM;
+    prm.sew    = fp; fp += BATCH*SEQ*DIM;
+    prm.gaw    = fp; fp += BATCH*SEQ*DIM;
+    prm.gbw    = fp; fp += BATCH*SEQ*DIM;
+
+    void* kargs[] = { (void*)&prm };
+    hipError_t cerr = hipLaunchCooperativeKernel((const void*)k_mega, dim3(256), dim3(256),
+                                                 kargs, 0, stream);
+    if (cerr != hipSuccess){
+        (void)hipGetLastError();
+        k_f_head<<<641, 256, 0, stream>>>(prm);
+        k_f_ab<<<640, 256, 0, stream>>>(prm);
+        k_f_dyn<<<1280, 256, 0, stream>>>(prm);
+        k_f_y<<<320, 256, 0, stream>>>(prm);
+        k_f_gcn<<<320, 256, 0, stream>>>(prm);
+        k_f_qkv<<<960, 256, 0, stream>>>(prm);
+        k_f_projattn<<<320, 256, 0, stream>>>(prm);
+        k_f_mlp1<<<1280, 256, 0, stream>>>(prm);
+        k_f_mlp2<<<640, 256, 0, stream>>>(prm);
+        k_f_gab<<<320, 256, 0, stream>>>(prm);
+        k_f_goutfin<<<320, 256, 0, stream>>>(prm);
+    }
+}
```
